# Performance work log

Hardware: AMD Instinct MI355X
Metric: run time of the kernel (lower is better)

Reference implementation:

```python
import jax, jax.numpy as jnp
import numpy as np

N_NODES = 50000
N_EDGES = 300000
H = 256
LN_EPS = 1e-5
NEG_SLOPE = 0.2  # PyG GATConv default


def layer_norm(x, g, b):
    mu = x.mean(-1, keepdims=True)
    var = ((x - mu) ** 2).mean(-1, keepdims=True)
    return (x - mu) * jax.lax.rsqrt(var + LN_EPS) * g + b


def gat_conv(x, src, dst, mask, W, a_src, a_dst, bias):
    # PyG GATConv(heads=1, concat=False) on the edge subset selected by `mask`,
    # with self-loops added for every node (PyG default add_self_loops=True).
    N = x.shape[0]
    h = x @ W                              # [N,H]
    s = h @ a_src                          # [N] alpha_src per node
    d = h @ a_dst                          # [N] alpha_dst per node
    e = jax.nn.leaky_relu(s[src] + d[dst], NEG_SLOPE)    # [E]
    e_masked = jnp.where(mask, e, -1e30)
    e_self = jax.nn.leaky_relu(s + d, NEG_SLOPE)         # [N] self-loop logits
    m = jnp.maximum(jax.ops.segment_max(e_masked, dst, num_segments=N), e_self)
    w = jnp.where(mask, jnp.exp(e - m[dst]), 0.0)        # masked edges -> 0
    w_self = jnp.exp(e_self - m)
    denom = jax.ops.segment_sum(w, dst, num_segments=N) + w_self
    num = jax.ops.segment_sum(w[:, None] * h[src], dst, num_segments=N) + w_self[:, None] * h
    return num / denom[:, None] + bias


def setup_inputs() -> dict:
    key = jax.random.key(0)
    ks = jax.random.split(key, 20)
    sc = 1.0 / np.sqrt(H)
    inp = {
        "x": jax.random.normal(ks[0], (N_NODES, H), jnp.float32),
        "edge_index": jax.random.randint(ks[1], (2, N_EDGES), 0, N_NODES, jnp.int64),
        "edge_attr": jax.random.randint(ks[2], (N_EDGES,), 0, 4, jnp.int64),
        # per-branch GATConv params (branches 0..2)
        "Wg": jax.random.normal(ks[3], (3, H, H), jnp.float32) * sc,
        "a_src": jax.random.normal(ks[4], (3, H), jnp.float32) * sc,
        "a_dst": jax.random.normal(ks[5], (3, H), jnp.float32) * sc,
        "bg": jnp.zeros((3, H), jnp.float32),
        # per-branch slice-strategy MLP: Linear + LayerNorm (+ReLU)
        "Ws": jax.random.normal(ks[6], (4, H, H), jnp.float32) * sc,
        "bs": jnp.zeros((4, H), jnp.float32),
        "gs": jnp.ones((4, H), jnp.float32),
        "betas": jnp.zeros((4, H), jnp.float32),
        # strategy selector MLP
        "W1": jax.random.normal(ks[7], (H, H // 2), jnp.float32) * sc,
        "b1": jnp.zeros((H // 2,), jnp.float32),
        "W2": jax.random.normal(ks[8], (H // 2, 4), jnp.float32) * (1.0 / np.sqrt(H // 2)),
        "b2": jnp.zeros((4,), jnp.float32),
        # fusion block
        "Wf": jax.random.normal(ks[9], (H, H), jnp.float32) * sc,
        "bf": jnp.zeros((H,), jnp.float32),
        "gf": jnp.ones((H,), jnp.float32),
        "betaf": jnp.zeros((H,), jnp.float32),
    }
    return inp


def reference(x, edge_index, edge_attr, Wg, a_src, a_dst, bg, Ws, bs, gs, betas,
              W1, b1, W2, b2, Wf, bf, gf, betaf):
    # strategy weights from mean graph representation (eval mode: dropout = identity)
    g = x.mean(axis=0)
    sw = jax.nn.softmax(jax.nn.relu(g @ W1 + b1) @ W2 + b2)  # [4]
    src, dst = edge_index[0], edge_index[1]
    combined = jnp.zeros_like(x)
    for i in range(4):
        if i < 3:
            xi = gat_conv(x, src, dst, edge_attr == i, Wg[i], a_src[i], a_dst[i], bg[i])
        else:
            xi = x
        si = jax.nn.relu(layer_norm(xi @ Ws[i] + bs[i], gs[i], betas[i]))
        combined = combined + si * sw[i]
    return jax.nn.relu(layer_norm(combined @ Wf + bf, gf, betaf))
```

## Files before the change

### kernel.cpp

```cpp
#include <hip/hip_runtime.h>

typedef unsigned short u16;
typedef short s16x8 __attribute__((ext_vector_type(8)));
typedef float f32x4 __attribute__((ext_vector_type(4)));
typedef u16 u16x4 __attribute__((ext_vector_type(4)));

#define NN 50000
#define NE 300000
#define HH 256
#define NCHUNK 196
#define NRC 98
#define NPB 12500

__device__ __forceinline__ float b2f(u16 u) {
  union { float f; unsigned int i; } v; v.i = ((unsigned int)u) << 16; return v.f;
}
__device__ __forceinline__ u16 f2b(float f) {
  union { float f; unsigned int i; } v; v.f = f;
  unsigned int u = v.i;
  unsigned int r = (u + 0x7fffu + ((u >> 16) & 1u)) >> 16;
  return (u16)r;
}
__device__ __forceinline__ float lrelu(float x) { return x > 0.f ? x : 0.2f * x; }

__device__ __forceinline__ int xcd_logical(int nwg) {
  int orig = blockIdx.x;
  int xcd = orig & 7, sl = orig >> 3;
  int q = nwg >> 3, r = nwg & 7;
  return (xcd < r) ? (xcd * (q + 1) + sl) : (r * (q + 1) + (xcd - r) * q + sl);
}

#define GLOAD_LDS16(SRC, DST)                                                   \
  __builtin_amdgcn_global_load_lds(                                             \
      (const __attribute__((address_space(1))) void*)(SRC),                     \
      (__attribute__((address_space(3))) void*)(DST), 16, 0, 0)

__device__ __forceinline__ f32x4 MFMA(s16x8 a, s16x8 b, f32x4 c) {
  return __builtin_amdgcn_mfma_f32_16x16x32_bf16(a, b, c, 0, 0, 0);
}

__device__ __forceinline__ void stageBhalf(const u16* __restrict__ BT, int half,
                                           char* lds, int lane, int wid) {
#pragma unroll
  for (int j = 0; j < 16; ++j) {
    int idx = j * 4 + wid;
    int q = idx >> 4, rem = idx & 15;
    int nf = rem >> 1, ks = rem & 1;
    int col = half * 128 + (lane & 15) * 8 + nf;
    GLOAD_LDS16((const char*)BT + col * 512 + q * 128 + ks * 64 + (lane >> 4) * 16,
                lds + idx * 1024);
  }
}

#define SGEMM_TILE(APTR, ASTRIDE, ACOLOFF)                                      \
  f32x4 acc[2][8] = {};                                                         \
  {                                                                             \
    s16x8 a[2][8];                                                              \
    const u16* a0p = (APTR) + (size_t)ar0 * (ASTRIDE) + (ACOLOFF) + cq8;        \
    const u16* a1p = (APTR) + (size_t)ar1 * (ASTRIDE) + (ACOLOFF) + cq8;        \
    _Pragma("unroll")                                                           \
    for (int ksp = 0; ksp < 8; ++ksp) {                                         \
      a[0][ksp] = *(const s16x8*)(a0p + ksp * 32);                              \
      a[1][ksp] = *(const s16x8*)(a1p + ksp * 32);                              \
    }                                                                           \
    _Pragma("unroll")                                                           \
    for (int ksp = 0; ksp < 8; ++ksp) {                                         \
      const char* bb = lds + (ksp >> 1) * 16384 + (ksp & 1) * 1024 + lane * 16; \
      _Pragma("unroll")                                                         \
      for (int nf = 0; nf < 8; ++nf) {                                          \
        s16x8 bf = *(const s16x8*)(bb + nf * 2048);                             \
        acc[0][nf] = MFMA(a[0][ksp], bf, acc[0][nf]);                           \
        acc[1][nf] = MFMA(a[1][ksp], bf, acc[1][nf]);                           \
      }                                                                         \
    }                                                                           \
  }

__global__ __launch_bounds__(256) void hgemm_s(
    const u16* __restrict__ xb, const u16* __restrict__ WT,
    const float* __restrict__ asrc, const float* __restrict__ adst,
    u16* __restrict__ h768, float* __restrict__ pSd, float* __restrict__ pDd,
    int M) {
  __shared__ __align__(16) char lds[65536];
  int cid = xcd_logical(6 * NRC);
  int rem = cid % 6, chunk = cid / 6;
  int b = rem >> 1, half = rem & 1;
  int tid = threadIdx.x, lane = tid & 63, wid = tid >> 6;
  int colL = lane & 15, cq = lane >> 4, cq8 = cq * 8;

  stageBhalf(WT + (size_t)b * 65536, half, lds, lane, wid);

  float a4[8], dd4[8];
#pragma unroll
  for (int nf = 0; nf < 8; ++nf) {
    int c = half * 128 + colL * 8 + nf;
    a4[nf] = asrc[b * 256 + c];
    dd4[nf] = adst[b * 256 + c];
  }
  float* st1 = pSd + (size_t)(b * 2 + half) * NN;
  float* st2 = pDd + (size_t)(b * 2 + half) * NN;
  __syncthreads();

  for (int rt = 0; rt < 4; ++rt) {
    int rowbase = chunk * 512 + rt * 128 + wid * 32;
    if (rowbase >= M) break;
    int ar0 = rowbase + colL; if (ar0 > M - 1) ar0 = M - 1;
    int ar1 = ar0 + 16; if (ar1 > M - 1) ar1 = M - 1;
    SGEMM_TILE(xb, 256, 0)
#pragma unroll
    for (int i = 0; i < 2; ++i)
#pragma unroll
      for (int r = 0; r < 4; ++r) {
        float sp = 0.f, dp = 0.f;
#pragma unroll
        for (int nf = 0; nf < 8; ++nf) {
          float v = acc[i][nf][r];
          sp += v * a4[nf]; dp += v * dd4[nf];
        }
#pragma unroll
        for (int m = 1; m < 16; m <<= 1) { sp += __shfl_xor(sp, m); dp += __shfl_xor(dp, m); }
        int row = rowbase + i * 16 + cq * 4 + r;
        if (row < M) {
          if (colL == 0) { st1[row] = sp; st2[row] = dp; }
          s16x8 o;
#pragma unroll
          for (int nf = 0; nf < 8; ++nf) o[nf] = (short)f2b(acc[i][nf][r]);
          *(s16x8*)(h768 + (size_t)row * 768 + b * 256 + half * 128 + colL * 8) = o;
        }
      }
  }
}

__global__ __launch_bounds__(256) void wsgemm_s(
    const u16* __restrict__ xiall, const u16* __restrict__ xb,
    const u16* __restrict__ WT, const float* __restrict__ bs,
    u16* __restrict__ y_raw, float* __restrict__ pS, float* __restrict__ pQ,
    int M) {
  __shared__ __align__(16) char lds[65536];
  int cid = xcd_logical(8 * NRC);
  int rem = cid & 7, chunk = cid >> 3;
  int b = rem >> 1, half = rem & 1;
  int tid = threadIdx.x, lane = tid & 63, wid = tid >> 6;
  int colL = lane & 15, cq = lane >> 4, cq8 = cq * 8;

  const u16* Ap = (b < 3) ? xiall : xb;
  int strideA = (b < 3) ? 768 : 256;
  int coloffA = (b < 3) ? b * 256 : 0;

  stageBhalf(WT + (size_t)(3 + b) * 65536, half, lds, lane, wid);

  float bv[8];
#pragma unroll
  for (int nf = 0; nf < 8; ++nf)
    bv[nf] = bs[b * 256 + half * 128 + colL * 8 + nf];
  float* st1 = pS + (size_t)(b * 2 + half) * NN;
  float* st2 = pQ + (size_t)(b * 2 + half) * NN;
  u16* yb = y_raw + (size_t)b * NN * 256;
  __syncthreads();

  for (int rt = 0; rt < 4; ++rt) {
    int rowbase = chunk * 512 + rt * 128 + wid * 32;
    if (rowbase >= M) break;
    int ar0 = rowbase + colL; if (ar0 > M - 1) ar0 = M - 1;
    int ar1 = ar0 + 16; if (ar1 > M - 1) ar1 = M - 1;
    SGEMM_TILE(Ap, strideA, coloffA)
#pragma unroll
    for (int i = 0; i < 2; ++i)
#pragma unroll
      for (int r = 0; r < 4; ++r) {
        float s = 0.f, q = 0.f;
#pragma unroll
        for (int nf = 0; nf < 8; ++nf) {
          float v = acc[i][nf][r] + bv[nf];
          acc[i][nf][r] = v;
          s += v; q += v * v;
        }
#pragma unroll
        for (int m = 1; m < 16; m <<= 1) { s += __shfl_xor(s, m); q += __shfl_xor(q, m); }
        int row = rowbase + i * 16 + cq * 4 + r;
        if (row < M) {
          if (colL == 0) { st1[row] = s; st2[row] = q; }
          s16x8 o;
#pragma unroll
          for (int nf = 0; nf < 8; ++nf) o[nf] = (short)f2b(acc[i][nf][r]);
          *(s16x8*)(yb + (size_t)row * 256 + half * 128 + colL * 8) = o;
        }
      }
  }
}

__global__ __launch_bounds__(256) void fingemm_s(
    const u16* __restrict__ comb, const u16* __restrict__ WT7,
    const float* __restrict__ bfv, u16* __restrict__ z_raw,
    float* __restrict__ pFS, float* __restrict__ pFQ, int M) {
  __shared__ __align__(16) char lds[65536];
  int cid = xcd_logical(2 * NRC);
  int half = cid & 1, chunk = cid >> 1;
  int tid = threadIdx.x, lane = tid & 63, wid = tid >> 6;
  int colL = lane & 15, cq = lane >> 4, cq8 = cq * 8;

  stageBhalf(WT7, half, lds, lane, wid);

  float bv[8];
#pragma unroll
  for (int nf = 0; nf < 8; ++nf)
    bv[nf] = bfv[half * 128 + colL * 8 + nf];
  float* st1 = pFS + (size_t)half * NN;
  float* st2 = pFQ + (size_t)half * NN;
  __syncthreads();

  for (int rt = 0; rt < 4; ++rt) {
    int rowbase = chunk * 512 + rt * 128 + wid * 32;
    if (rowbase >= M) break;
    int ar0 = rowbase + colL; if (ar0 > M - 1) ar0 = M - 1;
    int ar1 = ar0 + 16; if (ar1 > M - 1) ar1 = M - 1;
    SGEMM_TILE(comb, 256, 0)
#pragma unroll
    for (int i = 0; i < 2; ++i)
#pragma unroll
      for (int r = 0; r < 4; ++r) {
        float s = 0.f, q = 0.f;
#pragma unroll
        for (int nf = 0; nf < 8; ++nf) {
          float v = acc[i][nf][r] + bv[nf];
          acc[i][nf][r] = v;
          s += v; q += v * v;
        }
#pragma unroll
        for (int m = 1; m < 16; m <<= 1) { s += __shfl_xor(s, m); q += __shfl_xor(q, m); }
        int row = rowbase + i * 16 + cq * 4 + r;
        if (row < M) {
          if (colL == 0) { st1[row] = s; st2[row] = q; }
          s16x8 o;
#pragma unroll
          for (int nf = 0; nf < 8; ++nf) o[nf] = (short)f2b(acc[i][nf][r]);
          *(s16x8*)(z_raw + (size_t)row * 256 + half * 128 + colL * 8) = o;
        }
      }
  }
}

__global__ void sdfix(const float* __restrict__ pSd, const float* __restrict__ pDd,
                      float* __restrict__ s_arr, float* __restrict__ d_arr) {
  int i = blockIdx.x * 256 + threadIdx.x;
  if (i >= 3 * NN) return;
  int b = i / NN, v = i - b * NN;
  s_arr[i] = pSd[(size_t)(2 * b) * NN + v] + pSd[(size_t)(2 * b + 1) * NN + v];
  d_arr[i] = pDd[(size_t)(2 * b) * NN + v] + pDd[(size_t)(2 * b + 1) * NN + v];
}

__global__ void ln4(const u16* __restrict__ y_raw, const float* __restrict__ pS,
                    const float* __restrict__ pQ, const float* __restrict__ gs,
                    const float* __restrict__ betas, const float* __restrict__ sw,
                    u16* __restrict__ comb) {
  int v = blockIdx.x * 4 + (threadIdx.x >> 6);
  int lane = threadIdx.x & 63;
  int c0 = lane * 4;
  float accv[4] = {0.f, 0.f, 0.f, 0.f};
#pragma unroll
  for (int b = 0; b < 4; ++b) {
    float s = pS[(size_t)(2 * b) * NN + v] + pS[(size_t)(2 * b + 1) * NN + v];
    float q = pQ[(size_t)(2 * b) * NN + v] + pQ[(size_t)(2 * b + 1) * NN + v];
    float mu = s * (1.0f / HH);
    float var = q * (1.0f / HH) - mu * mu;
    float rs = rsqrtf(var + 1e-5f);
    float w = sw[b];
    u16x4 yv = *(const u16x4*)(y_raw + ((size_t)b * NN + v) * 256 + c0);
#pragma unroll
    for (int k = 0; k < 4; ++k) {
      float t = (b2f(yv[k]) - mu) * rs * gs[b * 256 + c0 + k] + betas[b * 256 + c0 + k];
      accv[k] += w * (t > 0.f ? t : 0.f);
    }
  }
  u16x4 o;
#pragma unroll
  for (int k = 0; k < 4; ++k) o[k] = f2b(accv[k]);
  *(u16x4*)(comb + (size_t)v * 256 + c0) = o;
}

__global__ void lnout(const u16* __restrict__ z_raw, const float* __restrict__ pFS,
                      const float* __restrict__ pFQ, const float* __restrict__ gf,
                      const float* __restrict__ betaf, float* __restrict__ outf) {
  int v = blockIdx.x * 4 + (threadIdx.x >> 6);
  int lane = threadIdx.x & 63;
  int c0 = lane * 4;
  float s = pFS[v] + pFS[(size_t)NN + v];
  float q = pFQ[v] + pFQ[(size_t)NN + v];
  float mu = s * (1.0f / HH);
  float var = q * (1.0f / HH) - mu * mu;
  float rs = rsqrtf(var + 1e-5f);
  u16x4 zv = *(const u16x4*)(z_raw + (size_t)v * 256 + c0);
  f32x4 o;
#pragma unroll
  for (int k = 0; k < 4; ++k) {
    float t = (b2f(zv[k]) - mu) * rs * gf[c0 + k] + betaf[c0 + k];
    o[k] = t > 0.f ? t : 0.f;
  }
  *(f32x4*)(outf + (size_t)v * 256 + c0) = o;
}

__global__ void xprep2(const float* __restrict__ x, u16* __restrict__ xb,
                       float* __restrict__ pg) {
  int tid = threadIdx.x, lane = tid & 63, w = tid >> 6;
  int r = blockIdx.x * 4 + w;
  f32x4 v = *(const f32x4*)(x + (size_t)r * HH + lane * 4);
  u16x4 o;
#pragma unroll
  for (int k = 0; k < 4; ++k) o[k] = f2b(v[k]);
  *(u16x4*)(xb + (size_t)r * HH + lane * 4) = o;
  __shared__ f32x4 sh[256];
  sh[tid] = v;
  __syncthreads();
  if (tid < 64) {
    f32x4 t = sh[tid] + sh[tid + 64] + sh[tid + 128] + sh[tid + 192];
    *(f32x4*)(pg + (size_t)blockIdx.x * 256 + lane * 4) = t;
  }
}

__global__ void gsum_red(const float* __restrict__ pg, float* __restrict__ g_sum) {
  int t = threadIdx.x;
  int r0 = blockIdx.x * 98;
  float s = 0.f;
  for (int r = r0; r < r0 + 98 && r < NPB; ++r) s += pg[(size_t)r * 256 + t];
  atomicAdd(&g_sum[t], s);
}

__global__ void transpose_all(const float* __restrict__ Wg, const float* __restrict__ Wsm,
                              const float* __restrict__ Wf, u16* __restrict__ WT) {
  __shared__ float tile[32][33];
  int z = blockIdx.z;
  const float* src = (z < 3) ? (Wg + (size_t)z * 65536)
                   : (z < 7) ? (Wsm + (size_t)(z - 3) * 65536) : Wf;
  u16* dst = WT + (size_t)z * 65536;
  int tx = threadIdx.x, ty = threadIdx.y;
  int bx = blockIdx.x, by = blockIdx.y;
#pragma unroll
  for (int j = 0; j < 32; j += 8)
    tile[ty + j][tx] = src[(size_t)(by * 32 + ty + j) * 256 + bx * 32 + tx];
  __syncthreads();
#pragma unroll
  for (int j = 0; j < 32; j += 8)
    dst[(size_t)(bx * 32 + ty + j) * 256 + by * 32 + tx] = f2b(tile[tx][ty + j]);
}

__global__ void selector_kernel(const float* __restrict__ g_sum,
                                const float* __restrict__ W1, const float* __restrict__ b1,
                                const float* __restrict__ W2, const float* __restrict__ b2,
                                float* __restrict__ sw) {
  __shared__ float gg[256];
  __shared__ float hid[128];
  __shared__ float lg[4];
  int t = threadIdx.x;
  gg[t] = g_sum[t] * (1.0f / NN);
  gg[t + 128] = g_sum[t + 128] * (1.0f / NN);
  __syncthreads();
  float a = 0.f;
  for (int c = 0; c < 256; ++c) a += gg[c] * W1[c * 128 + t];
  a += b1[t];
  hid[t] = a > 0.f ? a : 0.f;
  __syncthreads();
  if (t < 4) {
    float s = 0.f;
    for (int j = 0; j < 128; ++j) s += hid[j] * W2[j * 4 + t];
    lg[t] = s + b2[t];
  }
  __syncthreads();
  if (t == 0) {
    float m = fmaxf(fmaxf(lg[0], lg[1]), fmaxf(lg[2], lg[3]));
    float e0 = __expf(lg[0] - m), e1 = __expf(lg[1] - m);
    float e2 = __expf(lg[2] - m), e3 = __expf(lg[3] - m);
    float inv = 1.0f / (e0 + e1 + e2 + e3);
    sw[0] = e0 * inv; sw[1] = e1 * inv; sw[2] = e2 * inv; sw[3] = e3 * inv;
  }
}

__global__ void detect_kernel(const int* __restrict__ ei_raw, int* __restrict__ flag) {
  int t = threadIdx.x;
  int nz = 0;
  for (int k = t; k < 1024; k += 256) nz |= (ei_raw[2 * k + 1] != 0);
  if (nz) atomicOr(flag, 1);
}

__global__ void norm_edges(const int* __restrict__ ei_raw, const int* __restrict__ ea_raw,
                           const int* __restrict__ flag, int* __restrict__ srcE,
                           int* __restrict__ dstE, int* __restrict__ attrE) {
  int e = blockIdx.x * 256 + threadIdx.x;
  if (e >= NE) return;
  if (*flag) {
    srcE[e] = ei_raw[e];
    dstE[e] = ei_raw[NE + e];
    attrE[e] = ea_raw[e];
  } else {
    srcE[e] = ei_raw[2 * e];
    dstE[e] = ei_raw[2 * NE + 2 * e];
    attrE[e] = ea_raw[2 * e];
  }
}

__global__ void hist_kernel(const int* __restrict__ dstE, const int* __restrict__ attrE,
                            int* __restrict__ counts) {
  int e = blockIdx.x * 256 + threadIdx.x;
  if (e < NE) {
    int a = attrE[e];
    if ((unsigned)a < 3u) atomicAdd(&counts[a * NN + dstE[e]], 1);
  }
}

__global__ void scan1(const int* __restrict__ counts, int* __restrict__ offs,
                      int* __restrict__ bsum) {
  int b = blockIdx.y, c = blockIdx.x, t = threadIdx.x;
  int idx = c * 256 + t;
  int v = (idx < NN) ? counts[b * NN + idx] : 0;
  __shared__ int sh[256];
  sh[t] = v;
  __syncthreads();
  for (int o = 1; o < 256; o <<= 1) {
    int add = (t >= o) ? sh[t - o] : 0;
    __syncthreads();
    sh[t] += add;
    __syncthreads();
  }
  int incl = sh[t];
  if (idx < NN) offs[b * (NN + 1) + idx] = incl - v;
  if (t == 255) bsum[b * NCHUNK + c] = incl;
}

__global__ void scan2(const int* __restrict__ bsum, int* __restrict__ bpre,
                      int* __restrict__ offs) {
  int t = threadIdx.x;
  if (t < 3) {
    int run = 0;
    for (int c = 0; c < NCHUNK; ++c) { bpre[t * NCHUNK + c] = run; run += bsum[t * NCHUNK + c]; }
    offs[t * (NN + 1) + NN] = run;
  }
}

__global__ void scan3(const int* __restrict__ bpre, int* __restrict__ offs,
                      int* __restrict__ cur) {
  int b = blockIdx.y, c = blockIdx.x;
  int idx = c * 256 + threadIdx.x;
  if (idx < NN) {
    int val = offs[b * (NN + 1) + idx] + bpre[b * NCHUNK + c];
    offs[b * (NN + 1) + idx] = val;
    cur[b * NN + idx] = val;
  }
}

__global__ void scatter_kernel(const int* __restrict__ srcE, const int* __restrict__ dstE,
                               const int* __restrict__ attrE, int* __restrict__ cur,
                               int* __restrict__ elist) {
  int e = blockIdx.x * 256 + threadIdx.x;
  if (e < NE) {
    int a = attrE[e];
    if ((unsigned)a < 3u) {
      int p = atomicAdd(&cur[a * NN + dstE[e]], 1);
      elist[a * NE + p] = srcE[e];
    }
  }
}

__global__ void gat3(const int* __restrict__ offs, const int* __restrict__ elist,
                     const float* __restrict__ s_all, const float* __restrict__ d_all,
                     const u16* __restrict__ h, const float* __restrict__ bg,
                     u16* __restrict__ xiall) {
  int b = blockIdx.y;
  const int* offs_b = offs + (size_t)b * (NN + 1);
  const int* elist_b = elist + (size_t)b * NE;
  const float* s = s_all + (size_t)b * NN;
  const float* d = d_all + (size_t)b * NN;
  const float* bgrow = bg + b * 256;
  int v = blockIdx.x * 4 + (threadIdx.x >> 6);
  int lane = threadIdx.x & 63;
  float dv = d[v], sv = s[v];
  int beg = offs_b[v], end = offs_b[v + 1];
  float wself = __expf(lrelu(sv + dv));
  float denom = wself;
  float acc[4];
  u16x4 hv0 = *(const u16x4*)(h + (size_t)v * 768 + b * 256 + lane * 4);
#pragma unroll
  for (int k = 0; k < 4; ++k) acc[k] = wself * b2f(hv0[k]);
  for (int j = beg; j < end; ++j) {
    int u = elist_b[j];
    float w = __expf(lrelu(s[u] + dv));
    denom += w;
    u16x4 hv = *(const u16x4*)(h + (size_t)u * 768 + b * 256 + lane * 4);
#pragma unroll
    for (int k = 0; k < 4; ++k) acc[k] += w * b2f(hv[k]);
  }
  float inv = 1.0f / denom;
  f32x4 bg4 = *(const f32x4*)(bgrow + lane * 4);
  u16x4 outv;
#pragma unroll
  for (int k = 0; k < 4; ++k) outv[k] = f2b(acc[k] * inv + bg4[k]);
  *(u16x4*)(xiall + (size_t)v * 768 + b * 256 + lane * 4) = outv;
}

extern "C" void kernel_launch(void* const* d_in, const int* in_sizes, int n_in,
                              void* d_out, int out_size, void* d_ws, size_t ws_size,
                              hipStream_t stream) {
  const float* x   = (const float*)d_in[0];
  const int* ei    = (const int*)d_in[1];
  const int* ea    = (const int*)d_in[2];
  const float* Wg  = (const float*)d_in[3];
  const float* asrc= (const float*)d_in[4];
  const float* adst= (const float*)d_in[5];
  const float* bg  = (const float*)d_in[6];
  const float* Wsm = (const float*)d_in[7];
  const float* bs  = (const float*)d_in[8];
  const float* gs  = (const float*)d_in[9];
  const float* betas=(const float*)d_in[10];
  const float* W1  = (const float*)d_in[11];
  const float* b1  = (const float*)d_in[12];
  const float* W2  = (const float*)d_in[13];
  const float* b2  = (const float*)d_in[14];
  const float* Wf  = (const float*)d_in[15];
  const float* bfv = (const float*)d_in[16];
  const float* gf  = (const float*)d_in[17];
  const float* betaf=(const float*)d_in[18];
  float* out = (float*)d_out;

  char* wsb = (char*)d_ws;
  size_t off = 0;
  auto alloc = [&](size_t bytes) -> void* {
    void* p = wsb + off;
    off += bytes;
    off = (off + 255) & ~(size_t)255;
    return p;
  };
  int* flag    = (int*)alloc(sizeof(int));
  float* g_sum = (float*)alloc(256 * sizeof(float));
  float* sw    = (float*)alloc(4 * sizeof(float));
  int* counts  = (int*)alloc((size_t)3 * NN * sizeof(int));
  int* offs    = (int*)alloc((size_t)3 * (NN + 1) * sizeof(int));
  int* cur     = (int*)alloc((size_t)3 * NN * sizeof(int));
  int* bsum    = (int*)alloc((size_t)3 * NCHUNK * sizeof(int));
  int* bpre    = (int*)alloc((size_t)3 * NCHUNK * sizeof(int));
  int* srcE    = (int*)alloc((size_t)NE * sizeof(int));
  int* dstE    = (int*)alloc((size_t)NE * sizeof(int));
  int* attrE   = (int*)alloc((size_t)NE * sizeof(int));
  int* elist   = (int*)alloc((size_t)3 * NE * sizeof(int));
  float* s_arr = (float*)alloc((size_t)3 * NN * sizeof(float));
  float* d_arr = (float*)alloc((size_t)3 * NN * sizeof(float));
  float* pSd   = (float*)alloc((size_t)6 * NN * sizeof(float));
  float* pDd   = (float*)alloc((size_t)6 * NN * sizeof(float));
  float* pS    = (float*)alloc((size_t)8 * NN * sizeof(float));
  float* pQ    = (float*)alloc((size_t)8 * NN * sizeof(float));
  float* pFS   = (float*)alloc((size_t)2 * NN * sizeof(float));
  float* pFQ   = (float*)alloc((size_t)2 * NN * sizeof(float));
  float* pg    = (float*)alloc((size_t)NPB * 256 * sizeof(float));
  u16* WT      = (u16*)alloc((size_t)8 * 65536 * sizeof(u16));
  u16* xb      = (u16*)alloc((size_t)NN * HH * sizeof(u16));
  u16* h768    = (u16*)alloc((size_t)NN * 768 * sizeof(u16));
  u16* yb3     = (u16*)alloc((size_t)NN * 256 * sizeof(u16));
  u16* xiall   = (u16*)alloc((size_t)NN * 768 * sizeof(u16));
  u16* y_raw   = h768;
  u16* comb    = xiall;
  u16* z_raw   = xiall + (size_t)NN * 256;
  (void)yb3; (void)ws_size; (void)in_sizes; (void)n_in; (void)out_size;

  hipMemsetAsync(flag, 0, sizeof(int), stream);
  hipMemsetAsync(g_sum, 0, 256 * sizeof(float), stream);
  hipMemsetAsync(counts, 0, (size_t)3 * NN * sizeof(int), stream);

  detect_kernel<<<1, 256, 0, stream>>>(ei, flag);
  norm_edges<<<(NE + 255) / 256, 256, 0, stream>>>(ei, ea, flag, srcE, dstE, attrE);

  transpose_all<<<dim3(8, 8, 8), dim3(32, 8), 0, stream>>>(Wg, Wsm, Wf, WT);
  xprep2<<<NPB, 256, 0, stream>>>(x, xb, pg);
  gsum_red<<<128, 256, 0, stream>>>(pg, g_sum);
  selector_kernel<<<1, 128, 0, stream>>>(g_sum, W1, b1, W2, b2, sw);

  hist_kernel<<<(NE + 255) / 256, 256, 0, stream>>>(dstE, attrE, counts);
  scan1<<<dim3(NCHUNK, 3), 256, 0, stream>>>(counts, offs, bsum);
  scan2<<<1, 64, 0, stream>>>(bsum, bpre, offs);
  scan3<<<dim3(NCHUNK, 3), 256, 0, stream>>>(bpre, offs, cur);
  scatter_kernel<<<(NE + 255) / 256, 256, 0, stream>>>(srcE, dstE, attrE, cur, elist);

  hgemm_s<<<6 * NRC, 256, 0, stream>>>(xb, WT, asrc, adst, h768, pSd, pDd, NN);
  sdfix<<<(3 * NN + 255) / 256, 256, 0, stream>>>(pSd, pDd, s_arr, d_arr);
  gat3<<<dim3(12500, 3), 256, 0, stream>>>(offs, elist, s_arr, d_arr, h768, bg, xiall);
  wsgemm_s<<<8 * NRC, 256, 0, stream>>>(xiall, xb, WT, bs, y_raw, pS, pQ, NN);
  ln4<<<12500, 256, 0, stream>>>(y_raw, pS, pQ, gs, betas, sw, comb);
  fingemm_s<<<2 * NRC, 256, 0, stream>>>(comb, WT + (size_t)7 * 65536, bfv, z_raw, pFS, pFQ, NN);
  lnout<<<12500, 256, 0, stream>>>(z_raw, pFS, pFQ, gf, betaf, out);
}
```

Measured before the change: 341.0 us.

## Recompute branch GEMMs to fuse LayerNorm-ReLU-weighted-sum and drop y_raw buffer

Splits the per-branch slice GEMM into a stats-only pass that writes row sums and sums of squares, and an apply pass. The apply pass recomputes all four branch GEMMs per row tile and applies LayerNorm, ReLU and the strategy weighting in registers, writing only the combined bf16 tensor. This removes the large bf16 y_raw intermediate round trip and the separate ln4 kernel. In exchange it doubles the branch GEMM work and restages weights per branch within each block.

```diff
diff --git a/kernel.cpp b/kernel.cpp
--- a/kernel.cpp
+++ b/kernel.cpp
@@ -10,6 +10,7 @@
 #define HH 256
 #define NCHUNK 196
 #define NRC 98
+#define NCH2 391
 #define NPB 12500
 
 __device__ __forceinline__ float b2f(u16 u) {
@@ -130,11 +131,10 @@
   }
 }
 
-__global__ __launch_bounds__(256) void wsgemm_s(
+__global__ __launch_bounds__(256) void wsgemm_stats(
     const u16* __restrict__ xiall, const u16* __restrict__ xb,
     const u16* __restrict__ WT, const float* __restrict__ bs,
-    u16* __restrict__ y_raw, float* __restrict__ pS, float* __restrict__ pQ,
-    int M) {
+    float* __restrict__ pS, float* __restrict__ pQ, int M) {
   __shared__ __align__(16) char lds[65536];
   int cid = xcd_logical(8 * NRC);
   int rem = cid & 7, chunk = cid >> 3;
@@ -154,7 +154,6 @@
     bv[nf] = bs[b * 256 + half * 128 + colL * 8 + nf];
   float* st1 = pS + (size_t)(b * 2 + half) * NN;
   float* st2 = pQ + (size_t)(b * 2 + half) * NN;
-  u16* yb = y_raw + (size_t)b * NN * 256;
   __syncthreads();
 
   for (int rt = 0; rt < 4; ++rt) {
@@ -171,21 +170,84 @@
 #pragma unroll
         for (int nf = 0; nf < 8; ++nf) {
           float v = acc[i][nf][r] + bv[nf];
-          acc[i][nf][r] = v;
           s += v; q += v * v;
         }
 #pragma unroll
         for (int m = 1; m < 16; m <<= 1) { s += __shfl_xor(s, m); q += __shfl_xor(q, m); }
         int row = rowbase + i * 16 + cq * 4 + r;
-        if (row < M) {
-          if (colL == 0) { st1[row] = s; st2[row] = q; }
-          s16x8 o;
-#pragma unroll
-          for (int nf = 0; nf < 8; ++nf) o[nf] = (short)f2b(acc[i][nf][r]);
-          *(s16x8*)(yb + (size_t)row * 256 + half * 128 + colL * 8) = o;
+        if (colL == 0 && row < M) { st1[row] = s; st2[row] = q; }
+      }
+  }
+}
+
+__global__ __launch_bounds__(256) void wsapply(
+    const u16* __restrict__ xiall, const u16* __restrict__ xb,
+    const u16* __restrict__ WT, const float* __restrict__ bs,
+    const float* __restrict__ gs, const float* __restrict__ betas,
+    const float* __restrict__ sw, const float* __restrict__ pS,
+    const float* __restrict__ pQ, u16* __restrict__ comb, int M) {
+  __shared__ __align__(16) char lds[65536];
+  int cid = xcd_logical(2 * NCH2);
+  int half = cid & 1, chunk = cid >> 1;
+  int tid = threadIdx.x, lane = tid & 63, wid = tid >> 6;
+  int colL = lane & 15, cq = lane >> 4, cq8 = cq * 8;
+
+  int rowbase = chunk * 128 + wid * 32;
+  int ar0 = rowbase + colL; if (ar0 > M - 1) ar0 = M - 1;
+  int ar1 = ar0 + 16; if (ar1 > M - 1) ar1 = M - 1;
+
+  f32x4 cacc[2][8] = {};
+
+  for (int b = 0; b < 4; ++b) {
+    __syncthreads();
+    stageBhalf(WT + (size_t)(3 + b) * 65536, half, lds, lane, wid);
+
+    const u16* Ap = (b < 3) ? xiall : xb;
+    int strideA = (b < 3) ? 768 : 256;
+    int coloffA = (b < 3) ? b * 256 : 0;
+    float bv[8], g4[8], be4[8];
+#pragma unroll
+    for (int nf = 0; nf < 8; ++nf) {
+      int c = half * 128 + colL * 8 + nf;
+      bv[nf] = bs[b * 256 + c];
+      g4[nf] = gs[b * 256 + c];
+      be4[nf] = betas[b * 256 + c];
+    }
+    float w = sw[b];
+    __syncthreads();
+
+    SGEMM_TILE(Ap, strideA, coloffA)
+#pragma unroll
+    for (int i = 0; i < 2; ++i)
+#pragma unroll
+      for (int r = 0; r < 4; ++r) {
+        int row = rowbase + i * 16 + cq * 4 + r;
+        int rc = row < M ? row : M - 1;
+        float s = pS[(size_t)(2 * b) * NN + rc] + pS[(size_t)(2 * b + 1) * NN + rc];
+        float q = pQ[(size_t)(2 * b) * NN + rc] + pQ[(size_t)(2 * b + 1) * NN + rc];
+        float mu = s * (1.0f / HH);
+        float var = q * (1.0f / HH) - mu * mu;
+        float rs = rsqrtf(var + 1e-5f);
+#pragma unroll
+        for (int nf = 0; nf < 8; ++nf) {
+          float t = (acc[i][nf][r] + bv[nf] - mu) * rs * g4[nf] + be4[nf];
+          cacc[i][nf][r] += w * (t > 0.f ? t : 0.f);
         }
       }
   }
+
+#pragma unroll
+  for (int i = 0; i < 2; ++i)
+#pragma unroll
+    for (int r = 0; r < 4; ++r) {
+      int row = rowbase + i * 16 + cq * 4 + r;
+      if (row < M) {
+        s16x8 o;
+#pragma unroll
+        for (int nf = 0; nf < 8; ++nf) o[nf] = (short)f2b(cacc[i][nf][r]);
+        *(s16x8*)(comb + (size_t)row * 256 + half * 128 + colL * 8) = o;
+      }
+    }
 }
 
 __global__ __launch_bounds__(256) void fingemm_s(
@@ -246,35 +308,6 @@
   int b = i / NN, v = i - b * NN;
   s_arr[i] = pSd[(size_t)(2 * b) * NN + v] + pSd[(size_t)(2 * b + 1) * NN + v];
   d_arr[i] = pDd[(size_t)(2 * b) * NN + v] + pDd[(size_t)(2 * b + 1) * NN + v];
-}
-
-__global__ void ln4(const u16* __restrict__ y_raw, const float* __restrict__ pS,
-                    const float* __restrict__ pQ, const float* __restrict__ gs,
-                    const float* __restrict__ betas, const float* __restrict__ sw,
-                    u16* __restrict__ comb) {
-  int v = blockIdx.x * 4 + (threadIdx.x >> 6);
-  int lane = threadIdx.x & 63;
-  int c0 = lane * 4;
-  float accv[4] = {0.f, 0.f, 0.f, 0.f};
-#pragma unroll
-  for (int b = 0; b < 4; ++b) {
-    float s = pS[(size_t)(2 * b) * NN + v] + pS[(size_t)(2 * b + 1) * NN + v];
-    float q = pQ[(size_t)(2 * b) * NN + v] + pQ[(size_t)(2 * b + 1) * NN + v];
-    float mu = s * (1.0f / HH);
-    float var = q * (1.0f / HH) - mu * mu;
-    float rs = rsqrtf(var + 1e-5f);
-    float w = sw[b];
-    u16x4 yv = *(const u16x4*)(y_raw + ((size_t)b * NN + v) * 256 + c0);
-#pragma unroll
-    for (int k = 0; k < 4; ++k) {
-      float t = (b2f(yv[k]) - mu) * rs * gs[b * 256 + c0 + k] + betas[b * 256 + c0 + k];
-      accv[k] += w * (t > 0.f ? t : 0.f);
-    }
-  }
-  u16x4 o;
-#pragma unroll
-  for (int k = 0; k < 4; ++k) o[k] = f2b(accv[k]);
-  *(u16x4*)(comb + (size_t)v * 256 + c0) = o;
 }
 
 __global__ void lnout(const u16* __restrict__ z_raw, const float* __restrict__ pFS,
@@ -550,12 +583,10 @@
   u16* WT      = (u16*)alloc((size_t)8 * 65536 * sizeof(u16));
   u16* xb      = (u16*)alloc((size_t)NN * HH * sizeof(u16));
   u16* h768    = (u16*)alloc((size_t)NN * 768 * sizeof(u16));
-  u16* yb3     = (u16*)alloc((size_t)NN * 256 * sizeof(u16));
   u16* xiall   = (u16*)alloc((size_t)NN * 768 * sizeof(u16));
-  u16* y_raw   = h768;
-  u16* comb    = xiall;
-  u16* z_raw   = xiall + (size_t)NN * 256;
-  (void)yb3; (void)ws_size; (void)in_sizes; (void)n_in; (void)out_size;
+  u16* comb    = h768;
+  u16* z_raw   = xiall;
+  (void)ws_size; (void)in_sizes; (void)n_in; (void)out_size;
 
   hipMemsetAsync(flag, 0, sizeof(int), stream);
   hipMemsetAsync(g_sum, 0, 256 * sizeof(float), stream);
@@ -578,8 +609,8 @@
   hgemm_s<<<6 * NRC, 256, 0, stream>>>(xb, WT, asrc, adst, h768, pSd, pDd, NN);
   sdfix<<<(3 * NN + 255) / 256, 256, 0, stream>>>(pSd, pDd, s_arr, d_arr);
   gat3<<<dim3(12500, 3), 256, 0, stream>>>(offs, elist, s_arr, d_arr, h768, bg, xiall);
-  wsgemm_s<<<8 * NRC, 256, 0, stream>>>(xiall, xb, WT, bs, y_raw, pS, pQ, NN);
-  ln4<<<12500, 256, 0, stream>>>(y_raw, pS, pQ, gs, betas, sw, comb);
+  wsgemm_stats<<<8 * NRC, 256, 0, stream>>>(xiall, xb, WT, bs, pS, pQ, NN);
+  wsapply<<<2 * NCH2, 256, 0, stream>>>(xiall, xb, WT, bs, gs, betas, sw, pS, pQ, comb, NN);
   fingemm_s<<<2 * NRC, 256, 0, stream>>>(comb, WT + (size_t)7 * 65536, bfv, z_raw, pFS, pFQ, NN);
   lnout<<<12500, 256, 0, stream>>>(z_raw, pFS, pFQ, gf, betaf, out);
 }
```

Result: slower. 407.2 us (+19.4%).
